# Kernel tuning notes

Hardware: AMD Instinct MI355X
Metric: run time of the kernel (lower is better)

Reference implementation:

```python
import jax, jax.numpy as jnp
import numpy as np

THR_CONF = 0.5   # threshold_conf
THR_NMS = 0.3    # threshold_nms
K = 1024         # fixed pre-NMS top-k per image (jit-friendly stand-in for boolean filter)
VAR0, VAR1 = 0.1, 0.2  # SSD/RetinaFace decode variances


def setup_inputs() -> dict:
    key = jax.random.key(0)
    k1, k2, k3, k4 = jax.random.split(key, 4)
    B, N = 64, 16800
    p_loc = jax.random.normal(k1, (B, N, 4), jnp.float32)
    p_conf = jax.random.normal(k2, (B, N, 1), jnp.float32)
    p_landms = jax.random.normal(k3, (B, N, 10), jnp.float32)
    # anchor priors in cxcywh, normalized coords
    anchors = jax.random.uniform(k4, (N, 4), jnp.float32, 0.05, 0.6)
    return {"p_loc": p_loc, "p_conf": p_conf, "p_landms": p_landms, "anchors": anchors}


def _decode_boxes(anchors, loc):
    # fix_bbox: cxcy = a_cxcy + loc_xy * var0 * a_wh ; wh = a_wh * exp(loc_wh * var1)
    xy = anchors[..., :2] + loc[..., :2] * VAR0 * anchors[..., 2:]
    wh = anchors[..., 2:] * jnp.exp(loc[..., 2:] * VAR1)
    # xywh2ltrb
    return jnp.concatenate([xy - wh * 0.5, xy + wh * 0.5], axis=-1)  # (B,N,4)


def _decode_kpts(anchors, landms):
    # fix_keypoints: 5 points, each = a_cxcy + d * var0 * a_wh
    B, N, _ = landms.shape
    pts = landms.reshape(B, N, 5, 2)
    kp = anchors[:, None, :2] + pts * VAR0 * anchors[:, None, 2:]
    return kp.reshape(B, N, 10)


def _iou_matrix(b):  # b: (K,4) ltrb -> (K,K)
    area = jnp.maximum(b[:, 2] - b[:, 0], 0.0) * jnp.maximum(b[:, 3] - b[:, 1], 0.0)
    lt = jnp.maximum(b[:, None, :2], b[None, :, :2])
    rb = jnp.minimum(b[:, None, 2:], b[None, :, 2:])
    wh = jnp.maximum(rb - lt, 0.0)
    inter = wh[..., 0] * wh[..., 1]
    return inter / (area[:, None] + area[None, :] - inter + 1e-9)


def _nms_one(boxes, kpts, scores):
    # boxes (N,4), kpts (N,10), scores (N,)
    s = jnp.where(scores >= THR_CONF, scores, -1.0)  # conf mask
    vals, idx = jax.lax.top_k(s, K)                  # sorted candidates (torch nms sorts by score)
    b = boxes[idx]
    kp = kpts[idx]
    iou = _iou_matrix(b)
    ar = jnp.arange(K)

    def body(suppressed, i):
        keep_i = (vals[i] >= THR_CONF) & (~suppressed[i])
        suppressed = suppressed | (keep_i & (iou[i] > THR_NMS) & (ar > i))
        return suppressed, keep_i

    _, keep = jax.lax.scan(body, jnp.zeros(K, dtype=bool), ar)
    m = keep.astype(b.dtype)[:, None]
    # (K,15) = ltrb(4) | keypoints(10) | score(1), zeroed where suppressed/filtered
    return jnp.concatenate([b, kp, vals[:, None]], axis=-1) * m


def reference(p_loc, p_conf, p_landms, anchors):
    scores = jax.nn.sigmoid(p_conf)[..., 0]       # (B,N)
    boxes = _decode_boxes(anchors, p_loc)         # (B,N,4) ltrb
    kpts = _decode_kpts(anchors, p_landms)        # (B,N,10)
    return jax.vmap(_nms_one)(boxes, kpts, scores)  # (B,K,15)
```

## Files before the change

### kernel.cpp

```cpp
#include <hip/hip_runtime.h>
#include <cmath>

#define NB 64
#define NN 16800
#define KK 1024
#define NT 1024
#define CAP 2048
#define RQ 17

typedef unsigned long long ull;

__device__ __forceinline__ unsigned int score_key_f(float cf) {
  if (!(cf >= 0.0f)) return 0u;
  return (__float_as_uint(cf) & 0x7FFFFFFFu) + 1u;
}

__device__ __forceinline__ unsigned int bin_of_key(unsigned int key) {
  float cf = __uint_as_float(key - 1u);
  unsigned int bi = (unsigned int)(int)(cf * 1024.0f);
  return bi > 4095u ? 4095u : bi;
}

__device__ __forceinline__ ull score_key_d(float cf) {
  double s = 1.0 / (1.0 + exp(-(double)cf));
  if (!(s >= 0.5)) return 0ull;
  return ((ull)__double_as_longlong(s) & 0xFFFFFFFFFFFFFull) + 1ull;
}

__device__ __forceinline__ void decode_box_d(const float* lp, const float* ap,
                                             double& X0, double& Y0,
                                             double& X1, double& Y1,
                                             double& AR) {
#pragma clang fp contract(off)
  double l0 = (double)lp[0], l1 = (double)lp[1];
  double l2 = (double)lp[2], l3 = (double)lp[3];
  double a0 = (double)ap[0], a1 = (double)ap[1];
  double a2 = (double)ap[2], a3 = (double)ap[3];
  double xy0 = a0 + (l0 * 0.1) * a2;
  double xy1 = a1 + (l1 * 0.1) * a3;
  double w = a2 * exp(l2 * 0.2);
  double h = a3 * exp(l3 * 0.2);
  X0 = xy0 - w * 0.5; Y0 = xy1 - h * 0.5;
  X1 = xy0 + w * 0.5; Y1 = xy1 + h * 0.5;
  AR = fmax(X1 - X0, 0.0) * fmax(Y1 - Y0, 0.0);
}

__device__ __forceinline__ bool iou_gt_d(double i0, double i1, double i2,
                                         double i3, double ia, double j0,
                                         double j1, double j2, double j3,
                                         double ja) {
#pragma clang fp contract(off)
  double lt0 = fmax(i0, j0), lt1 = fmax(i1, j1);
  double rb0 = fmin(i2, j2), rb1 = fmin(i3, j3);
  double w0 = fmax(rb0 - lt0, 0.0), w1 = fmax(rb1 - lt1, 0.0);
  double inter = w0 * w1;
  double den = ((ia + ja) - inter) + 1e-9;
  return (inter / den) > 0.3;
}

__device__ __forceinline__ ull readlane64(ull v, int l) {
  unsigned int lo = __builtin_amdgcn_readlane((unsigned int)v, l);
  unsigned int hi = __builtin_amdgcn_readlane((unsigned int)(v >> 32), l);
  return ((ull)hi << 32) | (ull)lo;
}

__device__ __forceinline__ ull shfl64(ull v, int src) {
  unsigned int lo = (unsigned int)__shfl((int)(unsigned int)v, src);
  unsigned int hi = (unsigned int)__shfl((int)(unsigned int)(v >> 32), src);
  return ((ull)hi << 32) | (ull)lo;
}

__device__ __forceinline__ ull shflxor64(ull v, int m) {
  unsigned int lo = (unsigned int)__shfl_xor((int)(unsigned int)v, m);
  unsigned int hi = (unsigned int)__shfl_xor((int)(unsigned int)(v >> 32), m);
  return ((ull)hi << 32) | (ull)lo;
}

__global__ __launch_bounds__(1024, 1) void sort_kernel(
    const float* __restrict__ p_loc, const float* __restrict__ p_conf,
    const float* __restrict__ anchors, unsigned int* __restrict__ sidx_s,
    float* __restrict__ fbox, float* __restrict__ sval) {
  const int b = blockIdx.x;
  const int tid = threadIdx.x;
  const int lane = tid & 63;
  const int wave = tid >> 6;

  __shared__ unsigned int skey[CAP];
  __shared__ unsigned int sidx[CAP];
  __shared__ unsigned int hist[4096];
  __shared__ unsigned int base[4096];
  __shared__ unsigned int totals[64], chcarry[64];
  __shared__ unsigned int sh_found, sh_binT, sh_cB;
  __shared__ unsigned int scnt, sh_digit, sh_r, sh_c;

  const float* conf = p_conf + (size_t)b * NN;

  unsigned int rkey[RQ];
  #pragma unroll
  for (int q = 0; q < RQ; ++q) {
    const int i = tid + q * NT;
    rkey[q] = (i < NN) ? score_key_f(conf[i]) : 0u;
  }

  for (int i = tid; i < 4096; i += NT) hist[i] = 0u;
  if (tid == 0) sh_found = 0u;
  __syncthreads();
  #pragma unroll
  for (int q = 0; q < RQ; ++q) {
    unsigned int k = rkey[q];
    if (k != 0u) atomicAdd(&hist[bin_of_key(k)], 1u);
  }
  __syncthreads();
  for (int chunk = wave; chunk < 64; chunk += 16) {
    const int bin = chunk * 64 + (63 - lane);
    unsigned int c0 = hist[bin];
    unsigned int x = c0;
    #pragma unroll
    for (int d = 1; d < 64; d <<= 1) {
      unsigned int y = __shfl_up(x, d);
      if (lane >= d) x += y;
    }
    base[bin] = x;
    if (lane == 63) totals[chunk] = x;
  }
  __syncthreads();
  if (wave == 0) {
    const int chunk = 63 - lane;
    unsigned int t0 = totals[chunk];
    unsigned int x = t0;
    #pragma unroll
    for (int d = 1; d < 64; d <<= 1) {
      unsigned int y = __shfl_up(x, d);
      if (lane >= d) x += y;
    }
    chcarry[chunk] = x - t0;
  }
  __syncthreads();
  for (int chunk = wave; chunk < 64; chunk += 16) {
    const int bin = chunk * 64 + (63 - lane);
    unsigned int c0 = hist[bin];
    unsigned int S = chcarry[chunk] + base[bin] - c0;
    base[bin] = S;
    if (S < (unsigned)KK && (unsigned)KK <= S + c0) {
      sh_found = 1u; sh_binT = (unsigned int)bin; sh_cB = c0;
    }
  }
  __syncthreads();
  const bool fastOK = (sh_found != 0u) && (sh_cB <= 64u);
  const unsigned int binT = sh_binT;

  if (fastOK) {
    for (int i = tid; i < KK + 64; i += NT) { skey[i] = 0u; sidx[i] = 0xFFFFFFFFu; }
    __syncthreads();
    #pragma unroll
    for (int q = 0; q < RQ; ++q) {
      const int i = tid + q * NT;
      unsigned int k = rkey[q];
      if (k != 0u) {
        unsigned int bin = bin_of_key(k);
        if (bin >= binT) {
          unsigned int pos = atomicAdd(&base[bin], 1u);
          if (pos < (unsigned)(KK + 64)) { skey[pos] = k; sidx[pos] = (unsigned int)i; }
        }
      }
    }
    __syncthreads();
    for (int bin = (int)binT + tid; bin < 4096; bin += NT) {
      unsigned int cnt = hist[bin];
      if (cnt >= 2u) {
        int hi2 = (int)base[bin];
        int lo2 = hi2 - (int)cnt;
        for (int m2 = lo2 + 1; m2 < hi2; ++m2) {
          unsigned int kx = skey[m2]; unsigned int ix = sidx[m2];
          int n2 = m2;
          while (n2 > lo2) {
            unsigned int kp = skey[n2 - 1]; unsigned int ip = sidx[n2 - 1];
            bool after = (kp < kx) || (kp == kx && ip > ix);
            if (!after) break;
            skey[n2] = kp; sidx[n2] = ip; --n2;
          }
          skey[n2] = kx; sidx[n2] = ix;
        }
      }
    }
    __syncthreads();
  } else {
    unsigned int r = KK;
    unsigned int prefix = 0u, T = 0u;
    for (int pass = 0; pass < 4; ++pass) {
      const int shift = 24 - pass * 8;
      if (tid < 256) hist[tid] = 0u;
      __syncthreads();
      const unsigned int pm = pass ? ~((1u << (shift + 8)) - 1u) : 0u;
      #pragma unroll
      for (int q = 0; q < RQ; ++q) {
        unsigned int k = rkey[q];
        if (k != 0u && (k & pm) == prefix)
          atomicAdd(&hist[(k >> shift) & 255u], 1u);
      }
      __syncthreads();
      if (wave == 0) {
        if (lane == 0) { sh_digit = 0u; sh_r = r; sh_c = 0u; }
        unsigned int carry = 0;
        for (int chunk = 3; chunk >= 0; --chunk) {
          const int bin = chunk * 64 + (63 - lane);
          unsigned int c = hist[bin];
          unsigned int x = c;
          #pragma unroll
          for (int d = 1; d < 64; d <<= 1) {
            unsigned int y = __shfl_up(x, d);
            if (lane >= d) x += y;
          }
          unsigned int excl = x - c;
          unsigned int S = carry + excl;
          bool hit = (S < r) && (r <= S + c);
          ull bal = __ballot(hit ? 1 : 0);
          if (bal != 0ull) {
            int hl = __ffsll((long long)bal) - 1;
            unsigned int Sf = __shfl(S, hl);
            unsigned int bf = __shfl((unsigned int)bin, hl);
            unsigned int cf2 = __shfl(c, hl);
            if (lane == 0) { sh_digit = bf; sh_r = r - Sf; sh_c = cf2; }
            break;
          }
          carry += __shfl(x, 63);
        }
      }
      __syncthreads();
      prefix |= (sh_digit << shift);
      r = sh_r;
      const unsigned int cntge = (KK - r) + sh_c;
      if (cntge <= CAP || pass == 3) { T = prefix; break; }
    }

    if (tid == 0) scnt = 0u;
    for (int i = tid; i < CAP; i += NT) { skey[i] = 0u; sidx[i] = 0xFFFFFFFFu; }
    __syncthreads();
    #pragma unroll
    for (int q = 0; q < RQ; ++q) {
      const int i = tid + q * NT;
      unsigned int k = rkey[q];
      if (k != 0u && k >= T) {
        unsigned int pos = atomicAdd(&scnt, 1u);
        if (pos < CAP) { skey[pos] = k; sidx[pos] = (unsigned int)i; }
      }
    }
    __syncthreads();

    for (unsigned int k2 = 2; k2 <= CAP; k2 <<= 1) {
      for (unsigned int j = k2 >> 1; j > 0; j >>= 1) {
        for (int i = tid; i < CAP; i += NT) {
          int ixj = i ^ (int)j;
          if (ixj > i) {
            bool up = ((i & k2) == 0);
            unsigned int ka = skey[i], kbv = skey[ixj];
            unsigned int ia = sidx[i], ib = sidx[ixj];
            bool a_after_b = (ka < kbv) || (ka == kbv && ia > ib);
            if (a_after_b == up) {
              skey[i] = kbv; skey[ixj] = ka;
              sidx[i] = ib; sidx[ixj] = ia;
            }
          }
        }
        __syncthreads();
      }
    }
  }

  const unsigned int mykey = skey[tid];
  const unsigned int myidx = sidx[tid];
  double X0 = 0.0, Y0 = 0.0, X1 = 0.0, Y1 = 0.0, AR = 0.0;
  float v = -1.0f;
  if (mykey != 0u) {
    decode_box_d(p_loc + ((size_t)b * NN + myidx) * 4,
                 anchors + (size_t)myidx * 4, X0, Y0, X1, Y1, AR);
    double s = 1.0 / (1.0 + exp(-(double)conf[myidx]));
    v = (float)s;
  }
  sidx_s[(size_t)b * KK + tid] = myidx;
  float* fb = fbox + (size_t)b * 5 * KK;
  fb[0 * KK + tid] = (float)X0; fb[1 * KK + tid] = (float)Y0;
  fb[2 * KK + tid] = (float)X1; fb[3 * KK + tid] = (float)Y1;
  fb[4 * KK + tid] = (float)AR;
  sval[(size_t)b * KK + tid] = v;
}

__global__ __launch_bounds__(256) void pair_kernel(
    const float* __restrict__ p_loc, const float* __restrict__ anchors,
    const unsigned int* __restrict__ sidx_s, const float* __restrict__ fbox,
    const float* __restrict__ sval, ull* __restrict__ maskg) {
  const int img = blockIdx.x;
  const int wave = threadIdx.x >> 6;
  const int lane = threadIdx.x & 63;
  const int t = blockIdx.y * 4 + wave;

  int rg = 0, rem = t;
  while (rem >= 16 - rg) { rem -= 16 - rg; ++rg; }
  const int cg = rg + rem;

  const int rgs = __builtin_amdgcn_readfirstlane(rg);

  __shared__ float rowbuf[4][64][8];

  const float* fb = fbox + (size_t)img * 5 * KK;
  const int irow = rgs * 64 + lane;
  const int jcol = cg * 64 + lane;

  {
    const float v0 = fb[0 * KK + irow], v1 = fb[1 * KK + irow];
    const float v2 = fb[2 * KK + irow], v3 = fb[3 * KK + irow];
    const float va = fb[4 * KK + irow];
    float4* dst = reinterpret_cast<float4*>(&rowbuf[wave][lane][0]);
    *dst = make_float4(v0, v1, v2, v3);
    rowbuf[wave][lane][4] = va;
  }

  const unsigned int ri = sidx_s[(size_t)img * KK + irow];

  const float cj0 = fb[0 * KK + jcol], cj1 = fb[1 * KK + jcol];
  const float cj2 = fb[2 * KK + jcol], cj3 = fb[3 * KK + jcol];
  const float caj = fb[4 * KK + jcol];
  const unsigned int cidx = sidx_s[(size_t)img * KK + jcol];

  unsigned int wlo = 0u, whi = 0u;

  #pragma unroll 8
  for (int rr = 0; rr < 64; ++rr) {
    const float4 bq = *reinterpret_cast<const float4*>(&rowbuf[wave][rr][0]);
    const float ai = rowbuf[wave][rr][4];
    const float bi0 = bq.x, bi1 = bq.y, bi2 = bq.z, bi3 = bq.w;
    float lt0 = fmaxf(bi0, cj0), lt1 = fmaxf(bi1, cj1);
    float q0 = fminf(bi2, cj2), q1 = fminf(bi3, cj3);
    float w0 = fmaxf(q0 - lt0, 0.0f), w1 = fmaxf(q1 - lt1, 0.0f);
    float inter = w0 * w1;
    float den = ((ai + caj) - inter) + 1e-9f;
    float d = inter - 0.3f * den;
    bool bit = d > 0.0f;
    bool unc = fabsf(d) <= den * 1e-3f;
    if (__builtin_expect((bool)__ballot(unc ? 1 : 0), 0)) {
      const unsigned int rbi = __builtin_amdgcn_readlane(ri, rr);
      if (unc) {
        double rX0, rY0, rX1, rY1, rAR, qX0, qY0, qX1, qY1, qAR;
        decode_box_d(p_loc + ((size_t)img * NN + rbi) * 4,
                     anchors + (size_t)rbi * 4, rX0, rY0, rX1, rY1, rAR);
        decode_box_d(p_loc + ((size_t)img * NN + cidx) * 4,
                     anchors + (size_t)cidx * 4, qX0, qY0, qX1, qY1, qAR);
        bit = iou_gt_d(rX0, rY0, rX1, rY1, rAR, qX0, qY0, qX1, qY1, qAR);
      }
    }
    bit = bit && (jcol > rgs * 64 + rr);
    ull m = __ballot(bit ? 1 : 0);
    const bool mine = (lane == rr);
    wlo = mine ? (unsigned int)m : wlo;
    whi = mine ? (unsigned int)(m >> 32) : whi;
  }

  maskg[((size_t)img * KK + (size_t)rgs * 64 + lane) * 16 + cg] =
      ((ull)whi << 32) | (ull)wlo;
}

__global__ __launch_bounds__(1024, 1) void resolve_kernel(
    const float* __restrict__ p_landms, const float* __restrict__ anchors,
    const unsigned int* __restrict__ sidx_s, const float* __restrict__ fbox,
    const float* __restrict__ sval, const ull* __restrict__ maskg,
    float* __restrict__ out) {
  const int img = blockIdx.x, tid = threadIdx.x, lane = tid & 63,
            wave = tid >> 6;
  __shared__ ull buf[2][2048];
  __shared__ float svbuf[KK];
  __shared__ ull keepw[16];
  const ull* mg = maskg + (size_t)img * KK * 16;

  svbuf[tid] = sval[(size_t)img * KK + tid];
  for (int u = tid; u < 2048; u += NT) buf[0][u] = mg[u];
  __syncthreads();

  ull supw = 0ull;
  for (int s = 0; s < 8; ++s) {
    const int cur = s & 1;
    if (wave != 0) {
      if (s + 1 < 8) {
        const ull* src = mg + (size_t)(s + 1) * 2048;
        const int wmin = 2 * (s + 1);
        for (int u = tid - 64; u < 2048; u += NT - 64)
          if ((u & 15) >= wmin) buf[cur ^ 1][u] = src[u];
      }
    } else {
      #pragma unroll
      for (int half = 0; half < 2; ++half) {
        const int g = 2 * s + half;
        const ull vm = __ballot(svbuf[g * 64 + lane] >= 0.0f);
        const ull diagw = buf[cur][(half * 64 + lane) * 16 + g];
        ull curw = readlane64(supw, g);
        ull km = 0ull;
        #pragma unroll 8
        for (int rr = 0; rr < 64; ++rr) {
          const ull mw = readlane64(diagw, rr);
          const ull bitm = 1ull << rr;
          const ull keepbit = (vm & ~curw) & bitm;
          km |= keepbit;
          curw |= (keepbit != 0ull) ? mw : 0ull;
        }
        if (lane == 0) keepw[g] = km;
        if (g < 15) {
          const int w = lane >> 2, sub = lane & 3;
          ull acc = 0ull;
          #pragma unroll
          for (int t2 = 0; t2 < 16; ++t2) {
            const int rr = sub * 16 + t2;
            ull mv = buf[cur][(half * 64 + rr) * 16 + w];
            const ull kb = (km >> rr) & 1ull;
            acc |= (kb != 0ull) ? mv : 0ull;
          }
          if (w < g) acc = 0ull;
          acc |= shflxor64(acc, 1);
          acc |= shflxor64(acc, 2);
          const ull g4 = shfl64(acc, (lane & 15) * 4);
          if (lane < 16) supw |= g4;
          if (lane == g) supw = curw;
        }
      }
    }
    __syncthreads();
  }

  const bool keep = ((keepw[tid >> 6] >> (tid & 63)) & 1ull) != 0ull;
  float* op = out + ((size_t)img * KK + tid) * 15;
  if (keep) {
    const float* fb = fbox + (size_t)img * 5 * KK;
    op[0] = fb[0 * KK + tid]; op[1] = fb[1 * KK + tid];
    op[2] = fb[2 * KK + tid]; op[3] = fb[3 * KK + tid];
    const unsigned int myidx = sidx_s[(size_t)img * KK + tid];
    const float* pp = p_landms + ((size_t)img * NN + myidx) * 10;
    const float* ap = anchors + (size_t)myidx * 4;
    double a0 = (double)ap[0], a1 = (double)ap[1];
    double a2 = (double)ap[2], a3 = (double)ap[3];
    #pragma unroll
    for (int q = 0; q < 5; ++q) {
      double px = (double)pp[2 * q], py = (double)pp[2 * q + 1];
      op[4 + 2 * q]     = (float)(a0 + (px * 0.1) * a2);
      op[4 + 2 * q + 1] = (float)(a1 + (py * 0.1) * a3);
    }
    op[14] = svbuf[tid];
  } else {
    #pragma unroll
    for (int q = 0; q < 15; ++q) op[q] = 0.0f;
  }
}

__global__ __launch_bounds__(1024, 1) void fallback_kernel(
    const float* __restrict__ p_loc, const float* __restrict__ p_conf,
    const float* __restrict__ p_landms, const float* __restrict__ anchors,
    const ull* __restrict__ gkeys, float* __restrict__ out) {
  const int b = blockIdx.x;
  const int tid = threadIdx.x;
  const int lane = tid & 63;
  const int wave = tid >> 6;

  __shared__ ull skey[CAP];
  __shared__ unsigned int sidx[CAP];
  __shared__ float fb0[KK], fb1[KK], fb2[KK], fb3[KK], farr[KK];
  __shared__ float svalf[KK];
  __shared__ ull chunkmask[32][16];
  __shared__ unsigned int keepm[32];
  __shared__ ull supShared[16];
  __shared__ unsigned int hist[256];
  __shared__ unsigned int scnt, sh_digit, sh_r;

  unsigned long long rkey[RQ];
  if (gkeys != nullptr) {
    const ull* kb = gkeys + (size_t)b * NN;
    #pragma unroll
    for (int q = 0; q < RQ; ++q) {
      const int i = tid + q * NT;
      rkey[q] = (i < NN) ? kb[i] : 0ull;
    }
  } else {
    const float* conf = p_conf + (size_t)b * NN;
    #pragma unroll
    for (int q = 0; q < RQ; ++q) {
      const int i = tid + q * NT;
      rkey[q] = (i < NN) ? score_key_d(conf[i]) : 0ull;
    }
  }

  unsigned int r = KK;
  ull prefix = 0ull;
  for (int pass = 0; pass < 7; ++pass) {
    const int shift = 48 - pass * 8;
    if (tid < 256) hist[tid] = 0u;
    __syncthreads();
    const ull pm = (pass == 0) ? 0ull : ~((1ull << (shift + 8)) - 1ull);
    #pragma unroll
    for (int q = 0; q < RQ; ++q) {
      const int i = tid + q * NT;
      if (i < NN) {
        ull k = rkey[q];
        if (k != 0ull && (k & pm) == prefix)
          atomicAdd(&hist[(unsigned int)(k >> shift) & 255u], 1u);
      }
    }
    __syncthreads();
    if (wave == 0) {
      if (lane == 0) { sh_digit = 0u; sh_r = r; }
      unsigned int carry = 0;
      for (int chunk = 3; chunk >= 0; --chunk) {
        const int bin = chunk * 64 + (63 - lane);
        unsigned int c = hist[bin];
        unsigned int x = c;
        #pragma unroll
        for (int d = 1; d < 64; d <<= 1) {
          unsigned int y = __shfl_up(x, d);
          if (lane >= d) x += y;
        }
        unsigned int excl = x - c;
        unsigned int S = carry + excl;
        bool hit = (S < r) && (r <= S + c);
        ull bal = __ballot(hit ? 1 : 0);
        if (bal != 0ull) {
          int hl = __ffsll((long long)bal) - 1;
          unsigned int Sf = __shfl(S, hl);
          unsigned int bf = __shfl((unsigned int)bin, hl);
          if (lane == 0) { sh_digit = bf; sh_r = r - Sf; }
          break;
        }
        carry += __shfl(x, 63);
      }
    }
    __syncthreads();
    prefix |= ((ull)sh_digit << shift);
    r = sh_r;
    __syncthreads();
  }
  const ull T = prefix;

  if (tid == 0) scnt = 0u;
  for (int i = tid; i < CAP; i += NT) { skey[i] = 0ull; sidx[i] = 0xFFFFFFFFu; }
  __syncthreads();
  #pragma unroll
  for (int q = 0; q < RQ; ++q) {
    const int i = tid + q * NT;
    if (i < NN) {
      ull k = rkey[q];
      if (k != 0ull && k >= T) {
        unsigned int pos = atomicAdd(&scnt, 1u);
        if (pos < CAP) { skey[pos] = k; sidx[pos] = (unsigned int)i; }
      }
    }
  }
  __syncthreads();

  for (unsigned int k2 = 2; k2 <= CAP; k2 <<= 1) {
    for (unsigned int j = k2 >> 1; j > 0; j >>= 1) {
      for (int i = tid; i < CAP; i += NT) {
        int ixj = i ^ (int)j;
        if (ixj > i) {
          bool up = ((i & k2) == 0);
          ull ka = skey[i], kb = skey[ixj];
          unsigned int ia = sidx[i], ib = sidx[ixj];
          bool a_after_b = (ka < kb) || (ka == kb && ia > ib);
          if (a_after_b == up) {
            skey[i] = kb; skey[ixj] = ka;
            sidx[i] = ib; sidx[ixj] = ia;
          }
        }
      }
      __syncthreads();
    }
  }

  const ull mykey = skey[tid];
  const unsigned int myidx = sidx[tid];
  double dX0 = 0.0, dY0 = 0.0, dX1 = 0.0, dY1 = 0.0, dAR = 0.0;
  {
    float v = -1.0f;
    if (mykey != 0ull) {
      decode_box_d(p_loc + ((size_t)b * NN + myidx) * 4,
                   anchors + (size_t)myidx * 4, dX0, dY0, dX1, dY1, dAR);
      double s = __longlong_as_double(
          (long long)(0x3FE0000000000000ull | (mykey - 1ull)));
      v = (float)s;
    }
    fb0[tid] = (float)dX0; fb1[tid] = (float)dY0;
    fb2[tid] = (float)dX1; fb3[tid] = (float)dY1;
    farr[tid] = (float)dAR;
    svalf[tid] = v;
  }
  if (tid < 16) supShared[tid] = 0ull;
  if (tid < 32) keepm[tid] = 0u;
  __syncthreads();

  const float cj0 = fb0[tid], cj1 = fb1[tid], cj2 = fb2[tid], cj3 = fb3[tid];
  const float caj = farr[tid];
  ull supw = 0ull;

  for (int c = 0; c < 32; ++c) {
    for (int rr = 0; rr < 32; ++rr) {
      const int i = c * 32 + rr;
      const bool rowDead =
          (svalf[i] < 0.0f) ||
          (((supShared[i >> 6] >> (i & 63)) & 1ull) != 0ull);
      if (rowDead) continue;
      float bi0 = fb0[i], bi1 = fb1[i], bi2 = fb2[i], bi3 = fb3[i];
      float ai = farr[i];
      float lt0 = fmaxf(bi0, cj0), lt1 = fmaxf(bi1, cj1);
      float q0 = fminf(bi2, cj2), q1 = fminf(bi3, cj3);
      float w0 = fmaxf(q0 - lt0, 0.0f), w1 = fmaxf(q1 - lt1, 0.0f);
      float inter = w0 * w1;
      float den = ((ai + caj) - inter) + 1e-9f;
      float d = inter - 0.3f * den;
      bool bit = d > 0.0f;
      bool unc = fabsf(d) <= den * 1e-3f;
      if (__builtin_expect((bool)__ballot(unc ? 1 : 0), 0)) {
        if (unc) {
          const unsigned int ridx = sidx[i];
          double rX0, rY0, rX1, rY1, rAR;
          decode_box_d(p_loc + ((size_t)b * NN + ridx) * 4,
                       anchors + (size_t)ridx * 4, rX0, rY0, rX1, rY1, rAR);
          bit = iou_gt_d(rX0, rY0, rX1, rY1, rAR, dX0, dY0, dX1, dY1, dAR);
        }
      }
      bit = bit && (tid > i);
      ull m = __ballot(bit ? 1 : 0);
      if (lane == 0) chunkmask[rr][wave] = m;
    }
    __syncthreads();
    if (wave == 0) {
      unsigned int km = 0u;
      for (int rr = 0; rr < 32; ++rr) {
        const int i = c * 32 + rr;
        ull sc = __shfl(supw, i >> 6);
        bool keep = (svalf[i] >= 0.0f) && (((sc >> (i & 63)) & 1ull) == 0ull);
        if (keep) {
          km |= (1u << rr);
          if (lane < 16) supw |= chunkmask[rr][lane];
        }
      }
      if (lane == 0) keepm[c] = km;
      if (lane < 16) supShared[lane] = supw;
    }
    __syncthreads();
  }

  {
    const bool keep = ((keepm[tid >> 5] >> (tid & 31)) & 1u) != 0u;
    float* op = out + ((size_t)b * KK + tid) * 15;
    if (keep) {
      op[0] = fb0[tid]; op[1] = fb1[tid]; op[2] = fb2[tid]; op[3] = fb3[tid];
      const float* pp = p_landms + ((size_t)b * NN + myidx) * 10;
      const float* ap = anchors + (size_t)myidx * 4;
      double a0 = (double)ap[0], a1 = (double)ap[1];
      double a2 = (double)ap[2], a3 = (double)ap[3];
      #pragma unroll
      for (int q = 0; q < 5; ++q) {
        double px = (double)pp[2 * q], py = (double)pp[2 * q + 1];
        op[4 + 2 * q]     = (float)(a0 + (px * 0.1) * a2);
        op[4 + 2 * q + 1] = (float)(a1 + (py * 0.1) * a3);
      }
      op[14] = svalf[tid];
    } else {
      #pragma unroll
      for (int q = 0; q < 15; ++q) op[q] = 0.0f;
    }
  }
}

extern "C" void kernel_launch(void* const* d_in, const int* in_sizes, int n_in,
                              void* d_out, int out_size, void* d_ws, size_t ws_size,
                              hipStream_t stream) {
  const float* p_loc    = (const float*)d_in[0];
  const float* p_conf   = (const float*)d_in[1];
  const float* p_landms = (const float*)d_in[2];
  const float* anchors  = (const float*)d_in[3];
  float* out = (float*)d_out;
  (void)in_sizes; (void)n_in; (void)out_size;

  const size_t off_sidx = 0;
  const size_t off_fbox = off_sidx + (size_t)NB * KK * 4;
  const size_t off_sval = off_fbox + (size_t)NB * 5 * KK * 4;
  const size_t off_mask = off_sval + (size_t)NB * KK * 4;
  const size_t mask_bytes = (size_t)NB * KK * 16 * sizeof(ull);
  const size_t total = off_mask + mask_bytes;

  char* ws = (char*)d_ws;

  if (ws_size >= total) {
    unsigned int* sidx_s = (unsigned int*)(ws + off_sidx);
    float* fbox = (float*)(ws + off_fbox);
    float* sval = (float*)(ws + off_sval);
    ull* maskg = (ull*)(ws + off_mask);

    hipLaunchKernelGGL(sort_kernel, dim3(NB), dim3(NT), 0, stream,
                       p_loc, p_conf, anchors, sidx_s, fbox, sval);
    hipLaunchKernelGGL(pair_kernel, dim3(NB, 34), dim3(256), 0, stream,
                       p_loc, anchors, sidx_s, fbox, sval, maskg);
    hipLaunchKernelGGL(resolve_kernel, dim3(NB), dim3(NT), 0, stream,
                       p_landms, anchors, sidx_s, fbox, sval, maskg, out);
  } else {
    hipLaunchKernelGGL(fallback_kernel, dim3(NB), dim3(NT), 0, stream,
                       p_loc, p_conf, p_landms, anchors, (const ull*)nullptr,
                       out);
  }
}
```

Before: 197.6 us.

## Fuse NMS resolve into pair kernel via last-block-done atomic counter

Removes the separate resolve kernel launch. Each image's last-finishing pair block, found with a per-image atomic counter reset in the sort kernel, performs the greedy suppression scan and writes the output. The resolve now runs on a 256-thread block that reads mask words straight from global memory and combines suppression with LDS atomicOr, replacing the double-buffered LDS staging. It saves one launch and overlaps resolves across images, at the cost of fewer threads per resolve and more global-memory latency on the serial chain.

```diff
diff --git a/kernel.cpp b/kernel.cpp
--- a/kernel.cpp
+++ b/kernel.cpp
@@ -64,22 +64,11 @@
   return ((ull)hi << 32) | (ull)lo;
 }
 
-__device__ __forceinline__ ull shfl64(ull v, int src) {
-  unsigned int lo = (unsigned int)__shfl((int)(unsigned int)v, src);
-  unsigned int hi = (unsigned int)__shfl((int)(unsigned int)(v >> 32), src);
-  return ((ull)hi << 32) | (ull)lo;
-}
-
-__device__ __forceinline__ ull shflxor64(ull v, int m) {
-  unsigned int lo = (unsigned int)__shfl_xor((int)(unsigned int)v, m);
-  unsigned int hi = (unsigned int)__shfl_xor((int)(unsigned int)(v >> 32), m);
-  return ((ull)hi << 32) | (ull)lo;
-}
-
 __global__ __launch_bounds__(1024, 1) void sort_kernel(
     const float* __restrict__ p_loc, const float* __restrict__ p_conf,
     const float* __restrict__ anchors, unsigned int* __restrict__ sidx_s,
-    float* __restrict__ fbox, float* __restrict__ sval) {
+    float* __restrict__ fbox, float* __restrict__ sval,
+    unsigned int* __restrict__ done) {
   const int b = blockIdx.x;
   const int tid = threadIdx.x;
   const int lane = tid & 63;
@@ -92,6 +81,8 @@
   __shared__ unsigned int totals[64], chcarry[64];
   __shared__ unsigned int sh_found, sh_binT, sh_cB;
   __shared__ unsigned int scnt, sh_digit, sh_r, sh_c;
+
+  if (tid == 0) done[b] = 0u;
 
   const float* conf = p_conf + (size_t)b * NN;
 
@@ -285,13 +276,16 @@
   sval[(size_t)b * KK + tid] = v;
 }
 
-__global__ __launch_bounds__(256) void pair_kernel(
-    const float* __restrict__ p_loc, const float* __restrict__ anchors,
-    const unsigned int* __restrict__ sidx_s, const float* __restrict__ fbox,
-    const float* __restrict__ sval, ull* __restrict__ maskg) {
+__global__ __launch_bounds__(256, 8) void pair_kernel(
+    const float* __restrict__ p_loc, const float* __restrict__ p_landms,
+    const float* __restrict__ anchors, const unsigned int* __restrict__ sidx_s,
+    const float* __restrict__ fbox, const float* __restrict__ sval,
+    ull* __restrict__ maskg, unsigned int* __restrict__ done,
+    float* __restrict__ out) {
   const int img = blockIdx.x;
   const int wave = threadIdx.x >> 6;
   const int lane = threadIdx.x & 63;
+  const int tid = threadIdx.x;
   const int t = blockIdx.y * 4 + wave;
 
   int rg = 0, rem = t;
@@ -357,94 +351,93 @@
 
   maskg[((size_t)img * KK + (size_t)rgs * 64 + lane) * 16 + cg] =
       ((ull)whi << 32) | (ull)wlo;
-}
-
-__global__ __launch_bounds__(1024, 1) void resolve_kernel(
-    const float* __restrict__ p_landms, const float* __restrict__ anchors,
-    const unsigned int* __restrict__ sidx_s, const float* __restrict__ fbox,
-    const float* __restrict__ sval, const ull* __restrict__ maskg,
-    float* __restrict__ out) {
-  const int img = blockIdx.x, tid = threadIdx.x, lane = tid & 63,
-            wave = tid >> 6;
-  __shared__ ull buf[2][2048];
-  __shared__ float svbuf[KK];
-  __shared__ ull keepw[16];
+
+  __shared__ unsigned int sh_islast;
+  __threadfence();
+  __syncthreads();
+  if (tid == 0) {
+    const unsigned int old = atomicAdd(&done[img], 1u);
+    sh_islast = (old == 33u) ? 1u : 0u;
+  }
+  __syncthreads();
+  if (sh_islast == 0u) return;
+  __threadfence();
+
+  __shared__ ull vmw[16], supLDS[16], keepw16[16], kmsh;
   const ull* mg = maskg + (size_t)img * KK * 16;
 
-  svbuf[tid] = sval[(size_t)img * KK + tid];
-  for (int u = tid; u < 2048; u += NT) buf[0][u] = mg[u];
-  __syncthreads();
-
-  ull supw = 0ull;
-  for (int s = 0; s < 8; ++s) {
-    const int cur = s & 1;
-    if (wave != 0) {
-      if (s + 1 < 8) {
-        const ull* src = mg + (size_t)(s + 1) * 2048;
-        const int wmin = 2 * (s + 1);
-        for (int u = tid - 64; u < 2048; u += NT - 64)
-          if ((u & 15) >= wmin) buf[cur ^ 1][u] = src[u];
-      }
+  #pragma unroll
+  for (int k = 0; k < 4; ++k) {
+    const int g = wave * 4 + k;
+    const float v = sval[(size_t)img * KK + g * 64 + lane];
+    const ull vm = __ballot(v >= 0.0f);
+    if (lane == 0) vmw[g] = vm;
+  }
+  if (tid < 16) supLDS[tid] = 0ull;
+  __syncthreads();
+
+  ull diag_next = 0ull;
+  if (wave == 0) diag_next = mg[(size_t)lane * 16 + 0];
+  for (int g = 0; g < 16; ++g) {
+    if (wave == 0) {
+      const ull diagw = diag_next;
+      if (g < 15)
+        diag_next = mg[(size_t)((g + 1) * 64 + lane) * 16 + (g + 1)];
+      const ull vm = vmw[g];
+      ull curw = supLDS[g];
+      ull km = 0ull;
+      #pragma unroll 8
+      for (int rr = 0; rr < 64; ++rr) {
+        const ull mw = readlane64(diagw, rr);
+        const ull bitm = 1ull << rr;
+        const ull keepbit = (vm & ~curw) & bitm;
+        km |= keepbit;
+        curw |= (keepbit != 0ull) ? mw : 0ull;
+      }
+      if (lane == 0) { keepw16[g] = km; kmsh = km; }
+    }
+    __syncthreads();
+    if (g < 15) {
+      const ull km = kmsh;
+      const int w = tid >> 4, sub = tid & 15;
+      if (w > g) {
+        ull acc = 0ull;
+        #pragma unroll
+        for (int r2 = 0; r2 < 4; ++r2) {
+          const int rr = sub * 4 + r2;
+          if ((km >> rr) & 1ull)
+            acc |= mg[(size_t)(g * 64 + rr) * 16 + w];
+        }
+        if (acc != 0ull) atomicOr(&supLDS[w], acc);
+      }
+    }
+    __syncthreads();
+  }
+
+  #pragma unroll
+  for (int k = 0; k < 4; ++k) {
+    const int row = tid + k * 256;
+    const bool keep = ((keepw16[row >> 6] >> (row & 63)) & 1ull) != 0ull;
+    float* op = out + ((size_t)img * KK + row) * 15;
+    if (keep) {
+      op[0] = fb[0 * KK + row]; op[1] = fb[1 * KK + row];
+      op[2] = fb[2 * KK + row]; op[3] = fb[3 * KK + row];
+      const unsigned int myidx = sidx_s[(size_t)img * KK + row];
+      const float* pp = p_landms + ((size_t)img * NN + myidx) * 10;
+      const float* ap = anchors + (size_t)myidx * 4;
+      double a0 = (double)ap[0], a1 = (double)ap[1];
+      double a2 = (double)ap[2], a3 = (double)ap[3];
+      #pragma unroll
+      for (int q = 0; q < 5; ++q) {
+        double px = (double)pp[2 * q], py = (double)pp[2 * q + 1];
+        op[4 + 2 * q]     = (float)(a0 + (px * 0.1) * a2);
+        op[4 + 2 * q + 1] = (float)(a1 + (py * 0.1) * a3);
+      }
+      op[14] = sval[(size_t)img * KK + row];
     } else {
       #pragma unroll
-      for (int half = 0; half < 2; ++half) {
-        const int g = 2 * s + half;
-        const ull vm = __ballot(svbuf[g * 64 + lane] >= 0.0f);
-        const ull diagw = buf[cur][(half * 64 + lane) * 16 + g];
-        ull curw = readlane64(supw, g);
-        ull km = 0ull;
-        #pragma unroll 8
-        for (int rr = 0; rr < 64; ++rr) {
-          const ull mw = readlane64(diagw, rr);
-          const ull bitm = 1ull << rr;
-          const ull keepbit = (vm & ~curw) & bitm;
-          km |= keepbit;
-          curw |= (keepbit != 0ull) ? mw : 0ull;
-        }
-        if (lane == 0) keepw[g] = km;
-        if (g < 15) {
-          const int w = lane >> 2, sub = lane & 3;
-          ull acc = 0ull;
-          #pragma unroll
-          for (int t2 = 0; t2 < 16; ++t2) {
-            const int rr = sub * 16 + t2;
-            ull mv = buf[cur][(half * 64 + rr) * 16 + w];
-            const ull kb = (km >> rr) & 1ull;
-            acc |= (kb != 0ull) ? mv : 0ull;
-          }
-          if (w < g) acc = 0ull;
-          acc |= shflxor64(acc, 1);
-          acc |= shflxor64(acc, 2);
-          const ull g4 = shfl64(acc, (lane & 15) * 4);
-          if (lane < 16) supw |= g4;
-          if (lane == g) supw = curw;
-        }
-      }
-    }
-    __syncthreads();
-  }
-
-  const bool keep = ((keepw[tid >> 6] >> (tid & 63)) & 1ull) != 0ull;
-  float* op = out + ((size_t)img * KK + tid) * 15;
-  if (keep) {
-    const float* fb = fbox + (size_t)img * 5 * KK;
-    op[0] = fb[0 * KK + tid]; op[1] = fb[1 * KK + tid];
-    op[2] = fb[2 * KK + tid]; op[3] = fb[3 * KK + tid];
-    const unsigned int myidx = sidx_s[(size_t)img * KK + tid];
-    const float* pp = p_landms + ((size_t)img * NN + myidx) * 10;
-    const float* ap = anchors + (size_t)myidx * 4;
-    double a0 = (double)ap[0], a1 = (double)ap[1];
-    double a2 = (double)ap[2], a3 = (double)ap[3];
-    #pragma unroll
-    for (int q = 0; q < 5; ++q) {
-      double px = (double)pp[2 * q], py = (double)pp[2 * q + 1];
-      op[4 + 2 * q]     = (float)(a0 + (px * 0.1) * a2);
-      op[4 + 2 * q + 1] = (float)(a1 + (py * 0.1) * a3);
-    }
-    op[14] = svbuf[tid];
-  } else {
-    #pragma unroll
-    for (int q = 0; q < 15; ++q) op[q] = 0.0f;
+      for (int q = 0; q < 15; ++q) op[q] = 0.0f;
+    }
   }
 }
 
@@ -680,7 +673,8 @@
   const size_t off_sval = off_fbox + (size_t)NB * 5 * KK * 4;
   const size_t off_mask = off_sval + (size_t)NB * KK * 4;
   const size_t mask_bytes = (size_t)NB * KK * 16 * sizeof(ull);
-  const size_t total = off_mask + mask_bytes;
+  const size_t off_done = off_mask + mask_bytes;
+  const size_t total = off_done + NB * sizeof(unsigned int);
 
   char* ws = (char*)d_ws;
 
@@ -689,13 +683,13 @@
     float* fbox = (float*)(ws + off_fbox);
     float* sval = (float*)(ws + off_sval);
     ull* maskg = (ull*)(ws + off_mask);
+    unsigned int* done = (unsigned int*)(ws + off_done);
 
     hipLaunchKernelGGL(sort_kernel, dim3(NB), dim3(NT), 0, stream,
-                       p_loc, p_conf, anchors, sidx_s, fbox, sval);
+                       p_loc, p_conf, anchors, sidx_s, fbox, sval, done);
     hipLaunchKernelGGL(pair_kernel, dim3(NB, 34), dim3(256), 0, stream,
-                       p_loc, anchors, sidx_s, fbox, sval, maskg);
-    hipLaunchKernelGGL(resolve_kernel, dim3(NB), dim3(NT), 0, stream,
-                       p_landms, anchors, sidx_s, fbox, sval, maskg, out);
+                       p_loc, p_landms, anchors, sidx_s, fbox, sval, maskg,
+                       done, out);
   } else {
     hipLaunchKernelGGL(fallback_kernel, dim3(NB), dim3(NT), 0, stream,
                        p_loc, p_conf, p_landms, anchors, (const ull*)nullptr,
```

New measurement: 433.7 us. 119% more time.
